# Performance work log

Hardware: AMD Instinct MI355X
Metric: run time of the kernel (lower is better)

Reference implementation:

```python
import jax, jax.numpy as jnp
import numpy as np

B, S, D, H = 2, 2048, 1024, 16
HD = D // H  # head_dim = 64


def _rope_cos_sin(seq_len, head_dim, base=10000.0):
    # theta_i = base^(-2*(i-1)/dim), i = 1..dim/2
    i = jnp.arange(head_dim // 2, dtype=jnp.float32)
    theta = base ** (-2.0 * i / head_dim)
    m = jnp.arange(seq_len, dtype=jnp.float32)
    ang = jnp.outer(m, theta)  # [S, HD/2]
    return jnp.cos(ang), jnp.sin(ang)


def _apply_rope(x, cos, sin):
    # x: [B, S, H, HD]; pairs are consecutive elements (view_as_complex on (..., HD/2, 2))
    xr = x[..., 0::2]
    xi = x[..., 1::2]
    c = cos[None, :, None, :]
    s = sin[None, :, None, :]
    out_r = xr * c - xi * s
    out_i = xr * s + xi * c
    return jnp.stack([out_r, out_i], axis=-1).reshape(x.shape)


def setup_inputs() -> dict:
    key = jax.random.key(0)
    ks = jax.random.split(key, 7)
    sc = 1.0 / np.sqrt(D)
    return {
        "x": jax.random.normal(ks[0], (B, S, D), dtype=jnp.float32),
        "wq_w": jax.random.normal(ks[1], (D, D), dtype=jnp.float32) * sc,
        "wq_b": jax.random.normal(ks[2], (D,), dtype=jnp.float32) * 0.01,
        "wk_w": jax.random.normal(ks[3], (D, D), dtype=jnp.float32) * sc,
        "wk_b": jax.random.normal(ks[4], (D,), dtype=jnp.float32) * 0.01,
        "wv_w": jax.random.normal(ks[5], (D, D), dtype=jnp.float32) * sc,
        "wv_b": jax.random.normal(ks[6], (D,), dtype=jnp.float32) * 0.01,
    }


def reference(x, wq_w, wq_b, wk_w, wk_b, wv_w, wv_b):
    bs, seq_len, dim = x.shape
    # torch Linear: y = x @ W^T + b
    xq = (x @ wq_w.T + wq_b).reshape(bs, seq_len, H, HD)
    xk = (x @ wk_w.T + wk_b).reshape(bs, seq_len, H, HD)
    xv = (x @ wv_w.T + wv_b).reshape(bs, seq_len, H, HD)
    # RoPE (inference=True, start_pos=0): freqs for first seq_len positions
    cos, sin = _rope_cos_sin(seq_len, HD)
    xq = _apply_rope(xq, cos, sin)
    xk = _apply_rope(xk, cos, sin)
    # naive attention with full [B,H,S,S] score matrix, as in the original
    q = xq.transpose(0, 2, 1, 3)  # [B,H,S,HD]
    k = xk.transpose(0, 2, 1, 3)
    v = xv.transpose(0, 2, 1, 3)
    scores = jnp.einsum("bhqd,bhkd->bhqk", q, k) / np.sqrt(HD)
    attn = jax.nn.softmax(scores.astype(jnp.float32), axis=-1)
    out = jnp.einsum("bhqk,bhkd->bhqd", attn, v)
    return out.transpose(0, 2, 1, 3).reshape(bs, seq_len, dim)
```

## Files before the change

### kernel.cpp

```cpp
#include <hip/hip_runtime.h>


typedef __bf16 bf16;
typedef bf16  bf16x8 __attribute__((ext_vector_type(8)));
typedef bf16  bf16x4 __attribute__((ext_vector_type(4)));
typedef float f32x4  __attribute__((ext_vector_type(4)));
typedef float f32x16 __attribute__((ext_vector_type(16)));

typedef const __attribute__((address_space(1))) void* gptr_t;
typedef __attribute__((address_space(3))) void*       sptr_t;

__device__ __forceinline__ void gload_lds16(const void* g, void* l) {
  __builtin_amdgcn_global_load_lds((gptr_t)g, (sptr_t)l, 16, 0, 0);
}

__device__ __forceinline__ float fexp2(float x) {
  float r; asm("v_exp_f32 %0, %1" : "=v"(r) : "v"(x)); return r;
}
__device__ __forceinline__ float max3f(float a, float b, float c) {
  float r; asm("v_max3_f32 %0, %1, %2, %3" : "=v"(r) : "v"(a), "v"(b), "v"(c));
  return r;
}
__device__ __forceinline__ unsigned pkbf(float a, float b) {
  unsigned r;
  asm("v_cvt_pk_bf16_f32 %0, %1, %2" : "=v"(r) : "v"(a), "v"(b));
  return r;
}

__global__ __launch_bounds__(256) void prep_kernel(
    const float* __restrict__ x, const float* __restrict__ wq,
    const float* __restrict__ wk, const float* __restrict__ wv,
    bf16* __restrict__ xb, bf16* __restrict__ wqb, bf16* __restrict__ wkb,
    bf16* __restrict__ wvb, float* __restrict__ ctab, float* __restrict__ stab) {
  int g = blockIdx.x * 256 + threadIdx.x;
  const float* src;
  bf16* dst;
  int i;
  if (g < 1048576) { src = x; dst = xb; i = g; }
  else if (g < 1310720) { src = wq; dst = wqb; i = g - 1048576; }
  else if (g < 1572864) { src = wk; dst = wkb; i = g - 1310720; }
  else if (g < 1835008) { src = wv; dst = wvb; i = g - 1572864; }
  else {
    int idx = g - 1835008;
    if (idx < 65536) {
      int s = idx >> 5, p = idx & 31;
      double theta = exp2(-(double)p * (13.287712379549449 / 32.0));
      double ang = (double)s * theta;
      ctab[idx] = (float)cos(ang);
      stab[idx] = (float)sin(ang);
    }
    return;
  }
  const float4 v = reinterpret_cast<const float4*>(src)[i];
  bf16x4 o;
  o[0] = (bf16)v.x; o[1] = (bf16)v.y; o[2] = (bf16)v.z; o[3] = (bf16)v.w;
  reinterpret_cast<bf16x4*>(dst)[i] = o;
}

__global__ __launch_bounds__(256) void qkv_gemm_kernel(
    const bf16* __restrict__ xb, const bf16* __restrict__ wqb,
    const bf16* __restrict__ wkb, const bf16* __restrict__ wvb,
    const float* __restrict__ bq, const float* __restrict__ bk2,
    const float* __restrict__ bv, const float* __restrict__ ctab,
    const float* __restrict__ stab, bf16* __restrict__ qb,
    bf16* __restrict__ kb, bf16* __restrict__ vt) {
  const int z = blockIdx.z;
  const bf16* W = (z == 0) ? wqb : (z == 1) ? wkb : wvb;
  const float* bias = (z == 0) ? bq : (z == 1) ? bk2 : bv;

  __shared__ bf16 As[128 * 64];
  __shared__ bf16 Bs[128 * 64];

  const int tid = threadIdx.x;
  const int wid = tid >> 6;
  const int l = tid & 63;
  const int lg = l >> 4, lc = l & 15;
  const int wr = wid >> 1, wc = wid & 1;
  const int m0 = blockIdx.x * 128, n0 = blockIdx.y * 128;

  f32x4 acc[4][4] = {};

  const int srow = tid >> 3;
  const int schunk = (tid & 7) ^ (srow & 7);
  const bf16* asrc = xb + (size_t)(m0 + srow) * 1024 + schunk * 8;
  const bf16* bsrc = W + (size_t)(n0 + srow) * 1024 + schunk * 8;
  char* alds = (char*)As + wid * 1024;
  char* blds = (char*)Bs + wid * 1024;

  for (int k0 = 0; k0 < 1024; k0 += 64) {
#pragma unroll
    for (int i = 0; i < 4; ++i) {
      gload_lds16(asrc + (size_t)32 * i * 1024 + k0, alds + i * 4096);
      gload_lds16(bsrc + (size_t)32 * i * 1024 + k0, blds + i * 4096);
    }
    __syncthreads();
    bf16x8 af[4][2], bfr[4][2];
#pragma unroll
    for (int i = 0; i < 4; ++i) {
      const int row = wr * 64 + i * 16 + lc;
#pragma unroll
      for (int h = 0; h < 2; ++h) {
        const int slot = (h * 4 + lg) ^ (row & 7);
        af[i][h] = *reinterpret_cast<const bf16x8*>(
            (const char*)As + row * 128 + slot * 16);
      }
    }
#pragma unroll
    for (int j = 0; j < 4; ++j) {
      const int row = wc * 64 + j * 16 + lc;
#pragma unroll
      for (int h = 0; h < 2; ++h) {
        const int slot = (h * 4 + lg) ^ (row & 7);
        bfr[j][h] = *reinterpret_cast<const bf16x8*>(
            (const char*)Bs + row * 128 + slot * 16);
      }
    }
    __builtin_amdgcn_s_setprio(1);
#pragma unroll
    for (int i = 0; i < 4; ++i)
#pragma unroll
      for (int j = 0; j < 4; ++j) {
        acc[i][j] = __builtin_amdgcn_mfma_f32_16x16x32_bf16(af[i][0], bfr[j][0],
                                                            acc[i][j], 0, 0, 0);
        acc[i][j] = __builtin_amdgcn_mfma_f32_16x16x32_bf16(af[i][1], bfr[j][1],
                                                            acc[i][j], 0, 0, 0);
      }
    __builtin_amdgcn_s_setprio(0);
    __syncthreads();
  }

#pragma unroll
  for (int i = 0; i < 4; ++i)
#pragma unroll
    for (int j = 0; j < 4; ++j) {
      const int nb = n0 + wc * 64 + j * 16 + lc;
      const float bval = bias[nb];
#pragma unroll
      for (int r = 0; r < 4; ++r) {
        const int m = m0 + wr * 64 + i * 16 + lg * 4 + r;
        const float val = acc[i][j][r] + bval;
        if (z == 2) {
          vt[((size_t)((m >> 11) * 16 + (nb >> 6)) * 64 + (nb & 63)) * 2048 +
             (m & 2047)] = (bf16)val;
        } else {
          const int s = m & 2047;
          const int pi = (nb & 63) >> 1;
          const float c = ctab[s * 32 + pi];
          const float sn = stab[s * 32 + pi];
          const float part = __shfl_xor(val, 1, 64);
          float res = (nb & 1) ? fmaf(part, sn, val * c)
                               : fmaf(-part, sn, val * c);
          if (z == 0) res *= 0.18033688011112042f;
          bf16* dst = (z == 0) ? qb : kb;
          dst[(size_t)m * 1024 + nb] = (bf16)res;
        }
      }
    }
}

__device__ __forceinline__ void sm_pack(f32x16& s, float& mrun, float& lrun,
                                        f32x16& o0, f32x16& o1,
                                        const int sb, const int hi,
                                        unsigned* bu ) {
  float t0 = max3f(s[0], s[1], s[2]);
  float t1 = max3f(s[3], s[4], s[5]);
  float t2 = max3f(s[6], s[7], s[8]);
  float t3 = max3f(s[9], s[10], s[11]);
  float t4 = max3f(s[12], s[13], s[14]);
  float tm = fmaxf(max3f(t0, t1, t2), max3f(t3, t4, s[15]));
  tm = fmaxf(tm, __shfl_xor(tm, 32, 64));
  if (!__all(tm <= mrun + 8.0f)) {
    const float mn = fmaxf(mrun, tm);
    const float corr = fexp2(mrun - mn);
    mrun = mn;
    lrun *= corr;
#pragma unroll
    for (int r = 0; r < 16; ++r) { o0[r] *= corr; o1[r] *= corr; }
  }
  float ts = 0.f;
#pragma unroll
  for (int r = 0; r < 16; ++r) {
    s[r] = fexp2(s[r] - mrun);
    ts += s[r];
  }
  lrun += ts;

  unsigned pw[8];
#pragma unroll
  for (int w = 0; w < 8; ++w) pw[w] = pkbf(s[2 * w], s[2 * w + 1]);
  unsigned rx0 = __shfl_xor(pw[sb + 0], 32, 64);
  unsigned rx1 = __shfl_xor(pw[sb + 1], 32, 64);
  unsigned rx2 = __shfl_xor(pw[4 + sb + 0], 32, 64);
  unsigned rx3 = __shfl_xor(pw[4 + sb + 1], 32, 64);
  if (hi == 0) {
    bu[0] = pw[0]; bu[1] = pw[1]; bu[2] = rx0; bu[3] = rx1;
    bu[4] = pw[4]; bu[5] = pw[5]; bu[6] = rx2; bu[7] = rx3;
  } else {
    bu[0] = rx0; bu[1] = rx1; bu[2] = pw[2]; bu[3] = pw[3];
    bu[4] = rx2; bu[5] = rx3; bu[6] = pw[6]; bu[7] = pw[7];
  }
}

__global__ __launch_bounds__(128) void attn_kernel(const bf16* __restrict__ qb,
                                                   const bf16* __restrict__ kb,
                                                   const bf16* __restrict__ vt,
                                                   float* __restrict__ out) {
  __shared__ bf16 Kt[2][64][64];
  __shared__ bf16 Vt[2][64][64];

  const int tid = threadIdx.x;
  const int wid = tid >> 6;
  const int l = tid & 63;
  const int lc = l & 31;
  const int hi = l >> 5;
  const int bid = blockIdx.x;
  const int swz = (bid & 7) * 128 + (bid >> 3);
  const int bh = swz >> 5;
  const int qt = swz & 31;
  const int b = bh >> 4, h = bh & 15;
  const int q0 = qt * 64 + wid * 32;

  const bf16* Q = qb + (size_t)(b * 2048 + q0) * 1024 + h * 64;
  const bf16* K = kb + (size_t)(b * 2048) * 1024 + h * 64;
  const bf16* V = vt + (size_t)bh * 64 * 2048;

  bf16x8 qf[4];
#pragma unroll
  for (int md = 0; md < 4; ++md)
    qf[md] = *reinterpret_cast<const bf16x8*>(Q + (size_t)lc * 1024 + md * 16 + hi * 8);

  const int srow = l >> 3;
  const int schk = (l & 7) ^ (srow & 7);
  const bf16* ksrc = K + (size_t)(wid * 32 + srow) * 1024 + schk * 8;
  const bf16* vsrc = V + (size_t)(wid * 32 + srow) * 2048 + schk * 8;

  f32x16 o0 = {};
  f32x16 o1 = {};
  float mrun = -1e30f, lrun = 0.f;
  const int sb = (hi ^ 1) * 2;
  const int swzk = lc & 7;

#pragma unroll
  for (int j = 0; j < 4; ++j) {
    gload_lds16(ksrc + (size_t)8 * j * 1024, &Kt[0][wid * 32 + 8 * j][0]);
    gload_lds16(vsrc + (size_t)8 * j * 2048, &Vt[0][wid * 32 + 8 * j][0]);
  }
  __syncthreads();

  int bb = 0;
  for (int kt0 = 0; kt0 < 32; ++kt0) {
    if (kt0 < 31) {
      const size_t ko = (size_t)(kt0 + 1) * 64 * 1024;
      const size_t vo = (size_t)(kt0 + 1) * 64;
#pragma unroll
      for (int j = 0; j < 4; ++j) {
        gload_lds16(ksrc + ko + (size_t)8 * j * 1024,
                    &Kt[bb ^ 1][wid * 32 + 8 * j][0]);
        gload_lds16(vsrc + vo + (size_t)8 * j * 2048,
                    &Vt[bb ^ 1][wid * 32 + 8 * j][0]);
      }
    }

    bf16x8 kf0[4], kf1[4];
#pragma unroll
    for (int md = 0; md < 4; ++md) {
      const int slot = (((md << 1) | hi) ^ swzk) << 3;
      kf0[md] = *reinterpret_cast<const bf16x8*>(&Kt[bb][lc][slot]);
      kf1[md] = *reinterpret_cast<const bf16x8*>(&Kt[bb][32 + lc][slot]);
    }
    f32x16 s0 = {}, s1 = {};
    __builtin_amdgcn_s_setprio(1);
#pragma unroll
    for (int md = 0; md < 4; ++md) {
      s0 = __builtin_amdgcn_mfma_f32_32x32x16_bf16(kf0[md], qf[md], s0, 0, 0, 0);
      s1 = __builtin_amdgcn_mfma_f32_32x32x16_bf16(kf1[md], qf[md], s1, 0, 0, 0);
    }
    __builtin_amdgcn_s_setprio(0);

    bf16x8 va00 = *reinterpret_cast<const bf16x8*>(&Vt[bb][lc][(hi ^ swzk) << 3]);
    bf16x8 va01 = *reinterpret_cast<const bf16x8*>(&Vt[bb][lc][((hi + 2) ^ swzk) << 3]);
    bf16x8 va10 = *reinterpret_cast<const bf16x8*>(&Vt[bb][lc + 32][(hi ^ swzk) << 3]);
    bf16x8 va11 = *reinterpret_cast<const bf16x8*>(&Vt[bb][lc + 32][((hi + 2) ^ swzk) << 3]);

    unsigned buA[8];
    sm_pack(s0, mrun, lrun, o0, o1, sb, hi, buA);
    union { unsigned u[4]; bf16x8 v; } A0, A1;
    A0.u[0] = buA[0]; A0.u[1] = buA[1]; A0.u[2] = buA[2]; A0.u[3] = buA[3];
    A1.u[0] = buA[4]; A1.u[1] = buA[5]; A1.u[2] = buA[6]; A1.u[3] = buA[7];

    __builtin_amdgcn_s_setprio(1);
    o0 = __builtin_amdgcn_mfma_f32_32x32x16_bf16(va00, A0.v, o0, 0, 0, 0);
    o1 = __builtin_amdgcn_mfma_f32_32x32x16_bf16(va10, A0.v, o1, 0, 0, 0);
    o0 = __builtin_amdgcn_mfma_f32_32x32x16_bf16(va01, A1.v, o0, 0, 0, 0);
    o1 = __builtin_amdgcn_mfma_f32_32x32x16_bf16(va11, A1.v, o1, 0, 0, 0);
    __builtin_amdgcn_s_setprio(0);

    bf16x8 vb00 = *reinterpret_cast<const bf16x8*>(&Vt[bb][lc][((4 + hi) ^ swzk) << 3]);
    bf16x8 vb01 = *reinterpret_cast<const bf16x8*>(&Vt[bb][lc][((6 + hi) ^ swzk) << 3]);
    bf16x8 vb10 = *reinterpret_cast<const bf16x8*>(&Vt[bb][lc + 32][((4 + hi) ^ swzk) << 3]);
    bf16x8 vb11 = *reinterpret_cast<const bf16x8*>(&Vt[bb][lc + 32][((6 + hi) ^ swzk) << 3]);

    unsigned buB[8];
    sm_pack(s1, mrun, lrun, o0, o1, sb, hi, buB);
    union { unsigned u[4]; bf16x8 v; } B0, B1;
    B0.u[0] = buB[0]; B0.u[1] = buB[1]; B0.u[2] = buB[2]; B0.u[3] = buB[3];
    B1.u[0] = buB[4]; B1.u[1] = buB[5]; B1.u[2] = buB[6]; B1.u[3] = buB[7];

    __builtin_amdgcn_s_setprio(1);
    o0 = __builtin_amdgcn_mfma_f32_32x32x16_bf16(vb00, B0.v, o0, 0, 0, 0);
    o1 = __builtin_amdgcn_mfma_f32_32x32x16_bf16(vb10, B0.v, o1, 0, 0, 0);
    o0 = __builtin_amdgcn_mfma_f32_32x32x16_bf16(vb01, B1.v, o0, 0, 0, 0);
    o1 = __builtin_amdgcn_mfma_f32_32x32x16_bf16(vb11, B1.v, o1, 0, 0, 0);
    __builtin_amdgcn_s_setprio(0);

    __syncthreads();
    bb ^= 1;
  }

  lrun += __shfl_xor(lrun, 32, 64);
  const float inv = 1.f / lrun;
  float* orow = out + (size_t)(b * 2048 + q0 + lc) * 1024 + h * 64;
#pragma unroll
  for (int g = 0; g < 4; ++g) {
    f32x4 v0, v1;
#pragma unroll
    for (int e = 0; e < 4; ++e) { v0[e] = o0[g * 4 + e] * inv; v1[e] = o1[g * 4 + e] * inv; }
    *reinterpret_cast<f32x4*>(orow + g * 8 + 4 * hi) = v0;
    *reinterpret_cast<f32x4*>(orow + 32 + g * 8 + 4 * hi) = v1;
  }
}

extern "C" void kernel_launch(void* const* d_in, const int* in_sizes, int n_in,
                              void* d_out, int out_size, void* d_ws, size_t ws_size,
                              hipStream_t stream) {
  const float* x  = (const float*)d_in[0];
  const float* wq = (const float*)d_in[1];
  const float* bq = (const float*)d_in[2];
  const float* wk = (const float*)d_in[3];
  const float* bk = (const float*)d_in[4];
  const float* wv = (const float*)d_in[5];
  const float* bv = (const float*)d_in[6];
  float* out = (float*)d_out;

  char* ws = (char*)d_ws;
  bf16* xb  = (bf16*)(ws);
  bf16* wqb = (bf16*)(ws + 8388608);
  bf16* wkb = (bf16*)(ws + 10485760);
  bf16* wvb = (bf16*)(ws + 12582912);
  bf16* qb  = (bf16*)(ws + 14680064);
  bf16* kb  = (bf16*)(ws + 23068672);
  bf16* vt  = (bf16*)(ws + 31457280);
  float* ctab = (float*)(ws + 39845888);
  float* stab = (float*)(ws + 40108032);

  prep_kernel<<<7424, 256, 0, stream>>>(x, wq, wk, wv, xb, wqb, wkb, wvb,
                                        ctab, stab);

  qkv_gemm_kernel<<<dim3(32, 8, 3), 256, 0, stream>>>(
      xb, wqb, wkb, wvb, bq, bk, bv, ctab, stab, qb, kb, vt);

  attn_kernel<<<1024, 128, 0, stream>>>(qb, kb, vt, out);
}
```

Before: 213.5 us.

## Split KV range across wave pairs in attention and add separate V transpose kernel

The attention kernel now runs 256 threads per block. Two wave pairs each process half of the key sequence (split-K) for the same 64 query rows, and their partial softmax states are merged through LDS at the end. This raises waves per block and per-wave independence to improve latency hiding. In exchange it adds a reduction epilogue and extra LDS traffic. The V transpose moves out of the strided scatter in the GEMM epilogue into a dedicated LDS-tiled transpose kernel, which adds a launch and an extra pass over V.

```diff
diff --git a/kernel.cpp b/kernel.cpp
--- a/kernel.cpp
+++ b/kernel.cpp
@@ -63,7 +63,7 @@
     const float* __restrict__ bq, const float* __restrict__ bk2,
     const float* __restrict__ bv, const float* __restrict__ ctab,
     const float* __restrict__ stab, bf16* __restrict__ qb,
-    bf16* __restrict__ kb, bf16* __restrict__ vt) {
+    bf16* __restrict__ kb, bf16* __restrict__ vb) {
   const int z = blockIdx.z;
   const bf16* W = (z == 0) ? wqb : (z == 1) ? wkb : wvb;
   const float* bias = (z == 0) ? bq : (z == 1) ? bk2 : bv;
@@ -140,8 +140,7 @@
         const int m = m0 + wr * 64 + i * 16 + lg * 4 + r;
         const float val = acc[i][j][r] + bval;
         if (z == 2) {
-          vt[((size_t)((m >> 11) * 16 + (nb >> 6)) * 64 + (nb & 63)) * 2048 +
-             (m & 2047)] = (bf16)val;
+          vb[(size_t)m * 1024 + nb] = (bf16)val;
         } else {
           const int s = m & 2047;
           const int pi = (nb & 63) >> 1;
@@ -156,6 +155,25 @@
         }
       }
     }
+}
+
+__global__ __launch_bounds__(256) void vtrans_kernel(const bf16* __restrict__ vb,
+                                                     bf16* __restrict__ vt) {
+  __shared__ bf16 tile[64][65];
+  const int bh = blockIdx.y, b = bh >> 4, h = bh & 15;
+  const int s0 = blockIdx.x * 64;
+  const int t = threadIdx.x;
+#pragma unroll
+  for (int idx = t; idx < 4096; idx += 256) {
+    int r = idx >> 6, c = idx & 63;
+    tile[r][c] = vb[(size_t)(b * 2048 + s0 + r) * 1024 + h * 64 + c];
+  }
+  __syncthreads();
+#pragma unroll
+  for (int idx = t; idx < 4096; idx += 256) {
+    int d = idx >> 6, r = idx & 63;
+    vt[(size_t)(bh * 64 + d) * 2048 + s0 + r] = tile[r][d];
+  }
 }
 
 __device__ __forceinline__ void sm_pack(f32x16& s, float& mrun, float& lrun,
@@ -201,38 +219,49 @@
   }
 }
 
-__global__ __launch_bounds__(128) void attn_kernel(const bf16* __restrict__ qb,
-                                                   const bf16* __restrict__ kb,
-                                                   const bf16* __restrict__ vt,
-                                                   float* __restrict__ out) {
-  __shared__ bf16 Kt[2][64][64];
-  __shared__ bf16 Vt[2][64][64];
+__global__ __launch_bounds__(256, 4) void attn_kernel(
+    const bf16* __restrict__ qb, const bf16* __restrict__ kb,
+    const bf16* __restrict__ vt, float* __restrict__ out) {
+  __shared__ bf16 Klds[2][32][128];
+  __shared__ bf16 Vlds[2][64][64];
 
   const int tid = threadIdx.x;
   const int wid = tid >> 6;
   const int l = tid & 63;
   const int lc = l & 31;
   const int hi = l >> 5;
+  const int qw = wid & 1;
+  const int kvh = wid >> 1;
   const int bid = blockIdx.x;
   const int swz = (bid & 7) * 128 + (bid >> 3);
   const int bh = swz >> 5;
   const int qt = swz & 31;
   const int b = bh >> 4, h = bh & 15;
-  const int q0 = qt * 64 + wid * 32;
+  const int q0 = qt * 64 + qw * 32;
 
   const bf16* Q = qb + (size_t)(b * 2048 + q0) * 1024 + h * 64;
-  const bf16* K = kb + (size_t)(b * 2048) * 1024 + h * 64;
-  const bf16* V = vt + (size_t)bh * 64 * 2048;
+  const bf16* Kbase = kb + (size_t)(b * 2048) * 1024 + h * 64;
+  const bf16* Vbase = vt + (size_t)bh * 64 * 2048;
 
   bf16x8 qf[4];
 #pragma unroll
   for (int md = 0; md < 4; ++md)
     qf[md] = *reinterpret_cast<const bf16x8*>(Q + (size_t)lc * 1024 + md * 16 + hi * 8);
 
-  const int srow = l >> 3;
-  const int schk = (l & 7) ^ (srow & 7);
-  const bf16* ksrc = K + (size_t)(wid * 32 + srow) * 1024 + schk * 8;
-  const bf16* vsrc = V + (size_t)(wid * 32 + srow) * 2048 + schk * 8;
+  const int o16 = l * 16;
+  const bf16* ksrc[2];
+  const bf16* vsrc[2];
+#pragma unroll
+  for (int j = 0; j < 2; ++j) {
+    const int gk = wid * 2 + j;
+    const int krow = gk * 4 + (o16 >> 8);
+    const int khalf = (o16 >> 7) & 1;
+    const int kchunk = ((o16 >> 4) & 7) ^ (krow & 7);
+    ksrc[j] = Kbase + (size_t)(khalf * 1024 + krow) * 1024 + kchunk * 8;
+    const int d = gk * 8 + (o16 >> 7);
+    const int vlog = ((o16 >> 4) & 7) ^ (d & 7);
+    vsrc[j] = Vbase + (size_t)d * 2048 + (vlog >> 2) * 1024 + (vlog & 3) * 8;
+  }
 
   f32x16 o0 = {};
   f32x16 o1 = {};
@@ -241,52 +270,53 @@
   const int swzk = lc & 7;
 
 #pragma unroll
-  for (int j = 0; j < 4; ++j) {
-    gload_lds16(ksrc + (size_t)8 * j * 1024, &Kt[0][wid * 32 + 8 * j][0]);
-    gload_lds16(vsrc + (size_t)8 * j * 2048, &Vt[0][wid * 32 + 8 * j][0]);
+  for (int j = 0; j < 2; ++j) {
+    const int gk = wid * 2 + j;
+    gload_lds16(ksrc[j], &Klds[0][gk * 4][0]);
+    gload_lds16(vsrc[j], &Vlds[0][gk * 8][0]);
   }
   __syncthreads();
 
   int bb = 0;
-  for (int kt0 = 0; kt0 < 32; ++kt0) {
-    if (kt0 < 31) {
-      const size_t ko = (size_t)(kt0 + 1) * 64 * 1024;
-      const size_t vo = (size_t)(kt0 + 1) * 64;
-#pragma unroll
-      for (int j = 0; j < 4; ++j) {
-        gload_lds16(ksrc + ko + (size_t)8 * j * 1024,
-                    &Kt[bb ^ 1][wid * 32 + 8 * j][0]);
-        gload_lds16(vsrc + vo + (size_t)8 * j * 2048,
-                    &Vt[bb ^ 1][wid * 32 + 8 * j][0]);
-      }
-    }
-
-    bf16x8 kf0[4], kf1[4];
+  for (int t = 0; t < 32; ++t) {
+    if (t < 31) {
+      const size_t ko = (size_t)(t + 1) * 32 * 1024;
+      const size_t vo = (size_t)(t + 1) * 32;
+#pragma unroll
+      for (int j = 0; j < 2; ++j) {
+        const int gk = wid * 2 + j;
+        gload_lds16(ksrc[j] + ko, &Klds[bb ^ 1][gk * 4][0]);
+        gload_lds16(vsrc[j] + vo, &Vlds[bb ^ 1][gk * 8][0]);
+      }
+    }
+
+    f32x16 s = {};
+    __builtin_amdgcn_s_setprio(1);
 #pragma unroll
     for (int md = 0; md < 4; ++md) {
-      const int slot = (((md << 1) | hi) ^ swzk) << 3;
-      kf0[md] = *reinterpret_cast<const bf16x8*>(&Kt[bb][lc][slot]);
-      kf1[md] = *reinterpret_cast<const bf16x8*>(&Kt[bb][32 + lc][slot]);
-    }
-    f32x16 s0 = {}, s1 = {};
-    __builtin_amdgcn_s_setprio(1);
-#pragma unroll
-    for (int md = 0; md < 4; ++md) {
-      s0 = __builtin_amdgcn_mfma_f32_32x32x16_bf16(kf0[md], qf[md], s0, 0, 0, 0);
-      s1 = __builtin_amdgcn_mfma_f32_32x32x16_bf16(kf1[md], qf[md], s1, 0, 0, 0);
+      const int slot = (((md << 1) | hi) ^ swzk);
+      bf16x8 kf = *reinterpret_cast<const bf16x8*>(
+          &Klds[bb][lc][kvh * 64 + slot * 8]);
+      s = __builtin_amdgcn_mfma_f32_32x32x16_bf16(kf, qf[md], s, 0, 0, 0);
     }
     __builtin_amdgcn_s_setprio(0);
 
-    bf16x8 va00 = *reinterpret_cast<const bf16x8*>(&Vt[bb][lc][(hi ^ swzk) << 3]);
-    bf16x8 va01 = *reinterpret_cast<const bf16x8*>(&Vt[bb][lc][((hi + 2) ^ swzk) << 3]);
-    bf16x8 va10 = *reinterpret_cast<const bf16x8*>(&Vt[bb][lc + 32][(hi ^ swzk) << 3]);
-    bf16x8 va11 = *reinterpret_cast<const bf16x8*>(&Vt[bb][lc + 32][((hi + 2) ^ swzk) << 3]);
-
-    unsigned buA[8];
-    sm_pack(s0, mrun, lrun, o0, o1, sb, hi, buA);
+    const int c0 = (kvh * 4 + hi);
+    const int c1 = (kvh * 4 + 2 + hi);
+    bf16x8 va00 = *reinterpret_cast<const bf16x8*>(
+        &Vlds[bb][lc][(c0 ^ (lc & 7)) * 8]);
+    bf16x8 va01 = *reinterpret_cast<const bf16x8*>(
+        &Vlds[bb][lc][(c1 ^ (lc & 7)) * 8]);
+    bf16x8 va10 = *reinterpret_cast<const bf16x8*>(
+        &Vlds[bb][lc + 32][(c0 ^ ((lc + 32) & 7)) * 8]);
+    bf16x8 va11 = *reinterpret_cast<const bf16x8*>(
+        &Vlds[bb][lc + 32][(c1 ^ ((lc + 32) & 7)) * 8]);
+
+    unsigned bu[8];
+    sm_pack(s, mrun, lrun, o0, o1, sb, hi, bu);
     union { unsigned u[4]; bf16x8 v; } A0, A1;
-    A0.u[0] = buA[0]; A0.u[1] = buA[1]; A0.u[2] = buA[2]; A0.u[3] = buA[3];
-    A1.u[0] = buA[4]; A1.u[1] = buA[5]; A1.u[2] = buA[6]; A1.u[3] = buA[7];
+    A0.u[0] = bu[0]; A0.u[1] = bu[1]; A0.u[2] = bu[2]; A0.u[3] = bu[3];
+    A1.u[0] = bu[4]; A1.u[1] = bu[5]; A1.u[2] = bu[6]; A1.u[3] = bu[7];
 
     __builtin_amdgcn_s_setprio(1);
     o0 = __builtin_amdgcn_mfma_f32_32x32x16_bf16(va00, A0.v, o0, 0, 0, 0);
@@ -295,38 +325,41 @@
     o1 = __builtin_amdgcn_mfma_f32_32x32x16_bf16(va11, A1.v, o1, 0, 0, 0);
     __builtin_amdgcn_s_setprio(0);
 
-    bf16x8 vb00 = *reinterpret_cast<const bf16x8*>(&Vt[bb][lc][((4 + hi) ^ swzk) << 3]);
-    bf16x8 vb01 = *reinterpret_cast<const bf16x8*>(&Vt[bb][lc][((6 + hi) ^ swzk) << 3]);
-    bf16x8 vb10 = *reinterpret_cast<const bf16x8*>(&Vt[bb][lc + 32][((4 + hi) ^ swzk) << 3]);
-    bf16x8 vb11 = *reinterpret_cast<const bf16x8*>(&Vt[bb][lc + 32][((6 + hi) ^ swzk) << 3]);
-
-    unsigned buB[8];
-    sm_pack(s1, mrun, lrun, o0, o1, sb, hi, buB);
-    union { unsigned u[4]; bf16x8 v; } B0, B1;
-    B0.u[0] = buB[0]; B0.u[1] = buB[1]; B0.u[2] = buB[2]; B0.u[3] = buB[3];
-    B1.u[0] = buB[4]; B1.u[1] = buB[5]; B1.u[2] = buB[6]; B1.u[3] = buB[7];
-
-    __builtin_amdgcn_s_setprio(1);
-    o0 = __builtin_amdgcn_mfma_f32_32x32x16_bf16(vb00, B0.v, o0, 0, 0, 0);
-    o1 = __builtin_amdgcn_mfma_f32_32x32x16_bf16(vb10, B0.v, o1, 0, 0, 0);
-    o0 = __builtin_amdgcn_mfma_f32_32x32x16_bf16(vb01, B1.v, o0, 0, 0, 0);
-    o1 = __builtin_amdgcn_mfma_f32_32x32x16_bf16(vb11, B1.v, o1, 0, 0, 0);
-    __builtin_amdgcn_s_setprio(0);
-
     __syncthreads();
     bb ^= 1;
   }
 
-  lrun += __shfl_xor(lrun, 32, 64);
-  const float inv = 1.f / lrun;
-  float* orow = out + (size_t)(b * 2048 + q0 + lc) * 1024 + h * 64;
-#pragma unroll
-  for (int g = 0; g < 4; ++g) {
-    f32x4 v0, v1;
-#pragma unroll
-    for (int e = 0; e < 4; ++e) { v0[e] = o0[g * 4 + e] * inv; v1[e] = o1[g * 4 + e] * inv; }
-    *reinterpret_cast<f32x4*>(orow + g * 8 + 4 * hi) = v0;
-    *reinterpret_cast<f32x4*>(orow + 32 + g * 8 + 4 * hi) = v1;
+  float* c0lds = (float*)&Klds[0][0][0];
+  float* c1lds = (float*)&Vlds[0][0][0];
+  if (kvh == 1) {
+    float* d0 = c0lds + (qw * 64 + l) * 18;
+    float* d1 = c1lds + (qw * 64 + l) * 16;
+#pragma unroll
+    for (int r = 0; r < 16; ++r) { d0[r] = o0[r]; d1[r] = o1[r]; }
+    d0[16] = mrun; d0[17] = lrun;
+  }
+  __syncthreads();
+  if (kvh == 0) {
+    const float* s0 = c0lds + (qw * 64 + l) * 18;
+    const float* s1 = c1lds + (qw * 64 + l) * 16;
+    const float mb = s0[16], lb = s0[17];
+    const float M = fmaxf(mrun, mb);
+    const float ca = fexp2(mrun - M), cb = fexp2(mb - M);
+    lrun = lrun * ca + lb * cb;
+    lrun += __shfl_xor(lrun, 32, 64);
+    const float inv = 1.f / lrun;
+    float* orow = out + (size_t)(b * 2048 + q0 + lc) * 1024 + h * 64;
+#pragma unroll
+    for (int g = 0; g < 4; ++g) {
+      f32x4 v0, v1;
+#pragma unroll
+      for (int e = 0; e < 4; ++e) {
+        v0[e] = (o0[g * 4 + e] * ca + s0[g * 4 + e] * cb) * inv;
+        v1[e] = (o1[g * 4 + e] * ca + s1[g * 4 + e] * cb) * inv;
+      }
+      *reinterpret_cast<f32x4*>(orow + g * 8 + 4 * hi) = v0;
+      *reinterpret_cast<f32x4*>(orow + 32 + g * 8 + 4 * hi) = v1;
+    }
   }
 }
 
@@ -349,15 +382,18 @@
   bf16* wvb = (bf16*)(ws + 12582912);
   bf16* qb  = (bf16*)(ws + 14680064);
   bf16* kb  = (bf16*)(ws + 23068672);
-  bf16* vt  = (bf16*)(ws + 31457280);
-  float* ctab = (float*)(ws + 39845888);
-  float* stab = (float*)(ws + 40108032);
+  bf16* vb  = (bf16*)(ws + 31457280);
+  bf16* vt  = (bf16*)(ws + 39845888);
+  float* ctab = (float*)(ws + 48234496);
+  float* stab = (float*)(ws + 48496640);
 
   prep_kernel<<<7424, 256, 0, stream>>>(x, wq, wk, wv, xb, wqb, wkb, wvb,
                                         ctab, stab);
 
   qkv_gemm_kernel<<<dim3(32, 8, 3), 256, 0, stream>>>(
-      xb, wqb, wkb, wvb, bq, bk, bv, ctab, stab, qb, kb, vt);
-
-  attn_kernel<<<1024, 128, 0, stream>>>(qb, kb, vt, out);
-}
+      xb, wqb, wkb, wvb, bq, bk, bv, ctab, stab, qb, kb, vb);
+
+  vtrans_kernel<<<dim3(32, 32), 256, 0, stream>>>(vb, vt);
+
+  attn_kernel<<<1024, 256, 0, stream>>>(qb, kb, vt, out);
+}
```

Result: faster. 205.9 us (-3.6%).
